# Performance work log

Hardware: AMD Instinct MI355X
Metric: run time of the kernel (lower is better)

Reference implementation:

```python
import jax, jax.numpy as jnp
import numpy as np

K = 3        # kernel_size
STRIDE = 1
PAD = 1
DIL = 1


def setup_inputs() -> dict:
    key = jax.random.key(0)
    ks = jax.random.split(key, 5)
    B, C, H, W, O = 4, 64, 128, 128, 64
    x = jax.random.normal(ks[0], (B, C, H, W), jnp.float32)
    # small offset-conv weights -> offsets of a few pixels (realistic trained regime)
    offset_w = jax.random.normal(ks[1], (2 * K * K, C, K, K), jnp.float32) * 0.01
    offset_b = jax.random.normal(ks[2], (2 * K * K,), jnp.float32) * 0.01
    weight = jax.random.normal(ks[3], (O, C, K, K), jnp.float32)
    bias = jax.random.normal(ks[4], (O,), jnp.float32)
    return {"x": x, "offset_w": offset_w, "offset_b": offset_b,
            "weight": weight, "bias": bias}


def _conv2d(x, w, b):
    y = jax.lax.conv_general_dilated(
        x, w, window_strides=(STRIDE, STRIDE),
        padding=[(PAD, PAD), (PAD, PAD)],
        dimension_numbers=("NCHW", "OIHW", "NCHW"))
    return y + b[None, :, None, None]


def _deform_conv2d(x, offset, weight, bias):
    B, C, H, W = x.shape
    O = weight.shape[0]
    KK = K * K
    Ho, Wo = offset.shape[2], offset.shape[3]
    # offset channels ordered (y, x) per kernel tap: [B, KK, 2, Ho, Wo]
    off = offset.reshape(B, KK, 2, Ho, Wo)
    kyy, kxx = jnp.meshgrid(jnp.arange(K) * DIL, jnp.arange(K) * DIL, indexing="ij")
    kyy = kyy.reshape(KK).astype(x.dtype)
    kxx = kxx.reshape(KK).astype(x.dtype)
    base_y = (jnp.arange(Ho) * STRIDE - PAD).astype(x.dtype)
    base_x = (jnp.arange(Wo) * STRIDE - PAD).astype(x.dtype)
    # sampling positions [B, KK, Ho, Wo]
    py = base_y[None, None, :, None] + kyy[None, :, None, None] + off[:, :, 0]
    px = base_x[None, None, None, :] + kxx[None, :, None, None] + off[:, :, 1]

    y0 = jnp.floor(py); x0 = jnp.floor(px)
    y1 = y0 + 1.0;      x1 = x0 + 1.0
    wy1 = py - y0; wy0 = 1.0 - wy1
    wx1 = px - x0; wx0 = 1.0 - wx1

    xf = x.reshape(B, C, H * W)

    def corner(yc, xc):
        valid = (yc >= 0) & (yc < H) & (xc >= 0) & (xc < W)  # zero padding outside
        idx = (jnp.clip(yc, 0, H - 1) * W + jnp.clip(xc, 0, W - 1)).astype(jnp.int32)
        g = jax.vmap(lambda xb, ib: xb[:, ib.reshape(-1)])(xf, idx)  # [B, C, KK*Ho*Wo]
        g = g.reshape(B, C, KK, Ho, Wo)
        return g * valid[:, None].astype(x.dtype)

    val = (corner(y0, x0) * (wy0 * wx0)[:, None]
         + corner(y0, x1) * (wy0 * wx1)[:, None]
         + corner(y1, x0) * (wy1 * wx0)[:, None]
         + corner(y1, x1) * (wy1 * wx1)[:, None])  # [B, C, KK, Ho, Wo]

    out = jnp.einsum("bckhw,ock->bohw", val, weight.reshape(O, C, KK))
    return out + bias[None, :, None, None]


def reference(x, offset_w, offset_b, weight, bias):
    offset = _conv2d(x, offset_w, offset_b)
    return _deform_conv2d(x, offset, weight, bias)
```

## Files before the change

kernel.cpp:

```cpp
#include <hip/hip_runtime.h>

#define B_   4
#define C_   64
#define O_   64
#define H_   128
#define W_   128
#define HW_  (H_ * W_)
#define KK_  9
#define M_   18

typedef short  short8  __attribute__((ext_vector_type(8)));
typedef float  floatx4 __attribute__((ext_vector_type(4)));
typedef unsigned short ushort4v __attribute__((ext_vector_type(4)));
typedef unsigned short ushort8v __attribute__((ext_vector_type(8)));

static __device__ __forceinline__ unsigned short f2bf(float f) {
    unsigned int u = __float_as_uint(f);
    u += 0x7FFFu + ((u >> 16) & 1u);
    return (unsigned short)(u >> 16);
}
static __device__ __forceinline__ float bf2f(unsigned short s) {
    return __uint_as_float((unsigned int)s << 16);
}

__global__ __launch_bounds__(256) void prep(
        const float* __restrict__ x, const float* __restrict__ w,
        const float* __restrict__ ow, unsigned short* __restrict__ xT,
        unsigned short* __restrict__ wtbf, unsigned short* __restrict__ owtbf) {
    const int blk = blockIdx.x;
    if (blk < 512) {
        __shared__ unsigned short T[128][72];
        const int tid = threadIdx.x;
        const int y = blk & (H_ - 1);
        const int b = blk >> 7;
        const float* xby = x + (size_t)b * C_ * HW_ + y * W_;
        for (int i = tid; i < C_ * W_; i += 256) {
            const int c = i >> 7, xc = i & 127;
            T[xc][c] = f2bf(xby[(size_t)c * HW_ + xc]);
        }
        __syncthreads();
        unsigned short* dst = xT + (size_t)b * (4 * HW_ * 16) + y * (W_ * 16);
        for (int j = tid; j < 2048; j += 256) {
            const int g  = j >> 9;
            const int x8 = (j >> 2) & 127;
            const int c0 = (j & 3) * 4;
            const ushort4v pk = *(const ushort4v*)&T[x8][g * 16 + c0];
            *(ushort4v*)&dst[(size_t)g * (HW_ * 16) + x8 * 16 + c0] = pk;
        }
    } else if (blk < 530) {
        const int i = (blk - 512) * 256 + threadIdx.x;
        const int lane = i & 63, rest = i >> 6;
        const int ot = rest & 3, cks = rest >> 2;
        const int chunk = cks / 6, ks = cks % 6;
        const int o = ot * 16 + (lane & 15);
        const int kbase = chunk * 192 + ks * 32 + (lane >> 4) * 8;
        ushort8v pk;
        #pragma unroll
        for (int j = 0; j < 8; ++j) {
            const int k = kbase + j;
            pk[j] = f2bf(w[o * 576 + (k & 63) * 9 + (k >> 6)]);
        }
        *(ushort8v*)&wtbf[(size_t)i * 8] = pk;
    } else {
        const int i = (blk - 530) * 256 + threadIdx.x;
        const int lane = i & 63, rest = i >> 6;
        const int tile = rest & 1, tks = rest >> 1;
        const int tap = tks >> 1, ks = tks & 1;
        const int m = tile * 16 + (lane & 15);
        const int cb = ks * 32 + (lane >> 4) * 8;
        ushort8v pk;
        #pragma unroll
        for (int j = 0; j < 8; ++j)
            pk[j] = (m < M_) ? f2bf(ow[m * 576 + (cb + j) * 9 + tap])
                             : (unsigned short)0;
        *(ushort8v*)&owtbf[(size_t)i * 8] = pk;
    }
}

__global__ __launch_bounds__(256, 5) void dcn_fused(
        const unsigned short* __restrict__ xT,
        const unsigned short* __restrict__ owtbf, const float* __restrict__ ob,
        const unsigned short* __restrict__ wtbf, const float* __restrict__ bias,
        float* __restrict__ out) {
    __shared__ union {
        unsigned short P[3][66][72];
        struct {
            unsigned short vals[64][192];
            float offs[M_ * 64];
        } bv;
        float ep[4][16][65];
    } u;

    const int tid    = threadIdx.x;
    const int lane   = tid & 63;
    const int wslot  = __builtin_amdgcn_readfirstlane(tid >> 6);
    const int lane15 = lane & 15;
    const int quad   = lane >> 4;

    const int g    = blockIdx.x;
    const int xcd  = g & 7;
    const int slot = g >> 3;
    const int ho   = xcd * 16 + (slot >> 3);
    const int b    = (slot >> 1) & 3;
    const int wo_base = (slot & 1) << 6;

    const unsigned short* xTb = xT + (size_t)b * (4 * HW_ * 16);

    #pragma unroll
    for (int it = 0; it < 3; ++it) {
        const int t  = it * 4 + wslot;
        const int ky = t >> 2, cgp = t & 3;
        const int y  = ho - 1 + ky;
        const bool yv = (unsigned)y < (unsigned)H_;
        const unsigned short* src = xTb + (size_t)cgp * (HW_ * 16) + y * (W_ * 16);
        #pragma unroll
        for (int pass = 0; pass < 2; ++pass) {
            const int r = pass * 64 + lane;
            if (r < 66) {
                const int cx = wo_base + r - 1;
                ushort8v p0 = {0, 0, 0, 0, 0, 0, 0, 0};
                ushort8v p1 = {0, 0, 0, 0, 0, 0, 0, 0};
                if (yv && (unsigned)cx < (unsigned)W_) {
                    p0 = *(const ushort8v*)&src[cx * 16];
                    p1 = *(const ushort8v*)&src[cx * 16 + 8];
                }
                *(ushort8v*)&u.P[ky][r][cgp * 16]     = p0;
                *(ushort8v*)&u.P[ky][r][cgp * 16 + 8] = p1;
            }
        }
    }
    __syncthreads();

    {
        floatx4 oa0 = (floatx4){0.f, 0.f, 0.f, 0.f};
        floatx4 oa1 = (floatx4){0.f, 0.f, 0.f, 0.f};
        const int pxt = wslot;
        #pragma unroll
        for (int ky = 0; ky < 3; ++ky) {
            #pragma unroll
            for (int kx = 0; kx < 3; ++kx) {
                const int tap = ky * 3 + kx;
                #pragma unroll
                for (int ks = 0; ks < 2; ++ks) {
                    const int kk = ks * 32 + quad * 8;
                    const short8 af =
                        *(const short8*)&u.P[ky][pxt * 16 + lane15 + kx][kk];
                    const int fb = ((tap * 2 + ks) * 2) * 64 + lane;
                    const short8 bf0 = *(const short8*)&owtbf[(size_t)fb * 8];
                    const short8 bf1 =
                        *(const short8*)&owtbf[(size_t)(fb + 64) * 8];
                    oa0 = __builtin_amdgcn_mfma_f32_16x16x32_bf16(af, bf0, oa0, 0, 0, 0);
                    oa1 = __builtin_amdgcn_mfma_f32_16x16x32_bf16(af, bf1, oa1, 0, 0, 0);
                }
            }
        }
        __syncthreads();
        *(floatx4*)&u.bv.offs[lane15 * 64 + pxt * 16 + quad * 4] = oa0;
        if (lane15 < 2)
            *(floatx4*)&u.bv.offs[(16 + lane15) * 64 + pxt * 16 + quad * 4] = oa1;
    }
    __syncthreads();

    const int obase = wslot * 16;
    const int cg    = lane & 3;
    const int px16  = lane >> 2;
    floatx4 acc[4];
    #pragma unroll
    for (int t = 0; t < 4; ++t) acc[t] = (floatx4){0.f, 0.f, 0.f, 0.f};
    const unsigned short* xTw = xTb + (size_t)wslot * (HW_ * 16);

    for (int chunk = 0; chunk < 3; ++chunk) {
        #pragma unroll
        for (int tl = 0; tl < 3; ++tl) {
            const int k  = chunk * 3 + tl;
            const int ky = k / 3, kx = k % 3;
            const float oby = ob[2 * k], obx = ob[2 * k + 1];
            #pragma unroll
            for (int pxt = 0; pxt < 4; ++pxt) {
                const int px = pxt * 16 + px16;
                const float offy = u.bv.offs[(2 * k)     * 64 + px] + oby;
                const float offx = u.bv.offs[(2 * k + 1) * 64 + px] + obx;
                const float py  = (float)(ho - 1 + ky) + offy;
                const float pxx = (float)(wo_base - 1 + kx + px) + offx;
                const float fy = floorf(py), fx = floorf(pxx);
                const int y0 = (int)fy, x0 = (int)fx;
                const int y1 = y0 + 1,  x1 = x0 + 1;
                const float wy1 = py - fy,  wy0 = 1.f - wy1;
                const float wx1 = pxx - fx, wx0 = 1.f - wx1;
                const bool y0v = (unsigned)y0 < (unsigned)H_;
                const bool y1v = (unsigned)y1 < (unsigned)H_;
                const bool x0v = (unsigned)x0 < (unsigned)W_;
                const bool x1v = (unsigned)x1 < (unsigned)W_;
                const float w00 = (y0v && x0v) ? wy0 * wx0 : 0.f;
                const float w01 = (y0v && x1v) ? wy0 * wx1 : 0.f;
                const float w10 = (y1v && x0v) ? wy1 * wx0 : 0.f;
                const float w11 = (y1v && x1v) ? wy1 * wx1 : 0.f;
                const int ry0 = min(max(y0, 0), H_ - 1);
                const int ry1 = min(max(y1, 0), H_ - 1);
                const int cx0 = min(max(x0, 0), W_ - 1);
                const int cx1 = min(max(x1, 0), W_ - 1);
                const int a00 = (ry0 * W_ + cx0) * 16 + cg * 4;
                const int a01 = (ry0 * W_ + cx1) * 16 + cg * 4;
                const int a10 = (ry1 * W_ + cx0) * 16 + cg * 4;
                const int a11 = (ry1 * W_ + cx1) * 16 + cg * 4;
                const ushort4v q00 = *(const ushort4v*)&xTw[a00];
                const ushort4v q01 = *(const ushort4v*)&xTw[a01];
                const ushort4v q10 = *(const ushort4v*)&xTw[a10];
                const ushort4v q11 = *(const ushort4v*)&xTw[a11];
                ushort4v pk;
                #pragma unroll
                for (int q = 0; q < 4; ++q) {
                    const float val = bf2f(q00[q]) * w00 + bf2f(q01[q]) * w01
                                    + bf2f(q10[q]) * w10 + bf2f(q11[q]) * w11;
                    pk[q] = f2bf(val);
                }
                const int cidx =
                    tl * 8 + (((wslot << 1) + (cg >> 1)) ^ (px & 7));
                *(ushort4v*)&u.bv.vals[px][cidx * 8 + (cg & 1) * 4] = pk;
            }
        }
        __syncthreads();

        #pragma unroll
        for (int ks = 0; ks < 6; ++ks) {
            const short8 bfrag = *(const short8*)
                &wtbf[(size_t)(((chunk * 6 + ks) * 4 + wslot) * 64 + lane) * 8];
            const int ca  = (ks * 4 + quad) >> 3;
            const int cbr = ((ks * 4 + quad) & 7) ^ (lane15 & 7);
            #pragma unroll
            for (int t = 0; t < 4; ++t) {
                const int row = t * 16 + lane15;
                const short8 afrag =
                    *(const short8*)&u.bv.vals[row][(ca * 8 + cbr) * 8];
                acc[t] = __builtin_amdgcn_mfma_f32_16x16x32_bf16(
                             afrag, bfrag, acc[t], 0, 0, 0);
            }
        }
        __syncthreads();
    }

    #pragma unroll
    for (int t = 0; t < 4; ++t)
        #pragma unroll
        for (int r = 0; r < 4; ++r)
            u.ep[wslot][lane15][t * 16 + quad * 4 + r] = acc[t][r];
    __syncthreads();
    #pragma unroll
    for (int oi = 0; oi < 16; ++oi) {
        const int o = obase + oi;
        out[(size_t)(b * O_ + o) * HW_ + ho * W_ + wo_base + lane] =
            u.ep[wslot][oi][lane] + bias[o];
    }
}

extern "C" void kernel_launch(void* const* d_in, const int* in_sizes, int n_in,
                              void* d_out, int out_size, void* d_ws, size_t ws_size,
                              hipStream_t stream) {
    const float* x    = (const float*)d_in[0];
    const float* ow   = (const float*)d_in[1];
    const float* ob   = (const float*)d_in[2];
    const float* w    = (const float*)d_in[3];
    const float* bias = (const float*)d_in[4];
    float* out = (float*)d_out;

    unsigned short* wtbf  = (unsigned short*)d_ws;
    unsigned short* owtbf = wtbf + 4608 * 8;
    unsigned short* xT    = owtbf + 2304 * 8;

    prep<<<539, 256, 0, stream>>>(x, w, ow, xT, wtbf, owtbf);
    dcn_fused<<<B_ * H_ * (W_ / 64), 256, 0, stream>>>(xT, owtbf, ob, wtbf, bias, out);
}
```

Measured before the change: 117.9 us.

## Make each wave own a 16-pixel slice to drop inter-wave barriers

Reassigns the bilinear sampling and MFMA work so that each wavefront handles its own 16 output pixels across all 64 channels and all 64 output channels, instead of splitting work by channel group and output-channel group. The offsets, sampled values and epilogue staging then stay within a wave's private shared-memory rows, which removes most of the per-chunk __syncthreads barriers and the separate epilogue buffer. Offset bias is folded in once before the store. The launch bound drops from 5 to 4 waves per EU, and each wave now reads all four B-fragments from global memory per k-step, which raises global weight traffic and register pressure.

```diff
diff --git a/kernel.cpp b/kernel.cpp
--- a/kernel.cpp
+++ b/kernel.cpp
@@ -77,7 +77,7 @@
     }
 }
 
-__global__ __launch_bounds__(256, 5) void dcn_fused(
+__global__ __launch_bounds__(256, 4) void dcn_fused(
         const unsigned short* __restrict__ xT,
         const unsigned short* __restrict__ owtbf, const float* __restrict__ ob,
         const unsigned short* __restrict__ wtbf, const float* __restrict__ bias,
@@ -86,9 +86,8 @@
         unsigned short P[3][66][72];
         struct {
             unsigned short vals[64][192];
-            float offs[M_ * 64];
+            float offs[4][M_][16];
         } bv;
-        float ep[4][16][65];
     } u;
 
     const int tid    = threadIdx.x;
@@ -131,9 +130,9 @@
     }
     __syncthreads();
 
+    floatx4 oa0 = (floatx4){0.f, 0.f, 0.f, 0.f};
+    floatx4 oa1 = (floatx4){0.f, 0.f, 0.f, 0.f};
     {
-        floatx4 oa0 = (floatx4){0.f, 0.f, 0.f, 0.f};
-        floatx4 oa1 = (floatx4){0.f, 0.f, 0.f, 0.f};
         const int pxt = wslot;
         #pragma unroll
         for (int ky = 0; ky < 3; ++ky) {
@@ -154,59 +153,66 @@
                 }
             }
         }
-        __syncthreads();
-        *(floatx4*)&u.bv.offs[lane15 * 64 + pxt * 16 + quad * 4] = oa0;
-        if (lane15 < 2)
-            *(floatx4*)&u.bv.offs[(16 + lane15) * 64 + pxt * 16 + quad * 4] = oa1;
     }
     __syncthreads();
 
-    const int obase = wslot * 16;
-    const int cg    = lane & 3;
-    const int px16  = lane >> 2;
+    {
+        const float ob0 = ob[lane15];
+        #pragma unroll
+        for (int r = 0; r < 4; ++r) oa0[r] += ob0;
+        *(floatx4*)&u.bv.offs[wslot][lane15][quad * 4] = oa0;
+        if (lane15 < 2) {
+            const float ob1 = ob[16 + lane15];
+            #pragma unroll
+            for (int r = 0; r < 4; ++r) oa1[r] += ob1;
+            *(floatx4*)&u.bv.offs[wslot][16 + lane15][quad * 4] = oa1;
+        }
+    }
+
+    const int cg4  = lane & 3;
+    const int px16 = lane >> 2;
+    const int row  = wslot * 16 + px16;
     floatx4 acc[4];
     #pragma unroll
     for (int t = 0; t < 4; ++t) acc[t] = (floatx4){0.f, 0.f, 0.f, 0.f};
-    const unsigned short* xTw = xTb + (size_t)wslot * (HW_ * 16);
 
     for (int chunk = 0; chunk < 3; ++chunk) {
         #pragma unroll
         for (int tl = 0; tl < 3; ++tl) {
             const int k  = chunk * 3 + tl;
             const int ky = k / 3, kx = k % 3;
-            const float oby = ob[2 * k], obx = ob[2 * k + 1];
-            #pragma unroll
-            for (int pxt = 0; pxt < 4; ++pxt) {
-                const int px = pxt * 16 + px16;
-                const float offy = u.bv.offs[(2 * k)     * 64 + px] + oby;
-                const float offx = u.bv.offs[(2 * k + 1) * 64 + px] + obx;
-                const float py  = (float)(ho - 1 + ky) + offy;
-                const float pxx = (float)(wo_base - 1 + kx + px) + offx;
-                const float fy = floorf(py), fx = floorf(pxx);
-                const int y0 = (int)fy, x0 = (int)fx;
-                const int y1 = y0 + 1,  x1 = x0 + 1;
-                const float wy1 = py - fy,  wy0 = 1.f - wy1;
-                const float wx1 = pxx - fx, wx0 = 1.f - wx1;
-                const bool y0v = (unsigned)y0 < (unsigned)H_;
-                const bool y1v = (unsigned)y1 < (unsigned)H_;
-                const bool x0v = (unsigned)x0 < (unsigned)W_;
-                const bool x1v = (unsigned)x1 < (unsigned)W_;
-                const float w00 = (y0v && x0v) ? wy0 * wx0 : 0.f;
-                const float w01 = (y0v && x1v) ? wy0 * wx1 : 0.f;
-                const float w10 = (y1v && x0v) ? wy1 * wx0 : 0.f;
-                const float w11 = (y1v && x1v) ? wy1 * wx1 : 0.f;
-                const int ry0 = min(max(y0, 0), H_ - 1);
-                const int ry1 = min(max(y1, 0), H_ - 1);
-                const int cx0 = min(max(x0, 0), W_ - 1);
-                const int cx1 = min(max(x1, 0), W_ - 1);
-                const int a00 = (ry0 * W_ + cx0) * 16 + cg * 4;
-                const int a01 = (ry0 * W_ + cx1) * 16 + cg * 4;
-                const int a10 = (ry1 * W_ + cx0) * 16 + cg * 4;
-                const int a11 = (ry1 * W_ + cx1) * 16 + cg * 4;
-                const ushort4v q00 = *(const ushort4v*)&xTw[a00];
-                const ushort4v q01 = *(const ushort4v*)&xTw[a01];
-                const ushort4v q10 = *(const ushort4v*)&xTw[a10];
-                const ushort4v q11 = *(const ushort4v*)&xTw[a11];
+            const float offy = u.bv.offs[wslot][2 * k][px16];
+            const float offx = u.bv.offs[wslot][2 * k + 1][px16];
+            const float py  = (float)(ho - 1 + ky) + offy;
+            const float pxx = (float)(wo_base - 1 + kx + wslot * 16 + px16) + offx;
+            const float fy = floorf(py), fx = floorf(pxx);
+            const int y0 = (int)fy, x0 = (int)fx;
+            const int y1 = y0 + 1,  x1 = x0 + 1;
+            const float wy1 = py - fy,  wy0 = 1.f - wy1;
+            const float wx1 = pxx - fx, wx0 = 1.f - wx1;
+            const bool y0v = (unsigned)y0 < (unsigned)H_;
+            const bool y1v = (unsigned)y1 < (unsigned)H_;
+            const bool x0v = (unsigned)x0 < (unsigned)W_;
+            const bool x1v = (unsigned)x1 < (unsigned)W_;
+            const float w00 = (y0v && x0v) ? wy0 * wx0 : 0.f;
+            const float w01 = (y0v && x1v) ? wy0 * wx1 : 0.f;
+            const float w10 = (y1v && x0v) ? wy1 * wx0 : 0.f;
+            const float w11 = (y1v && x1v) ? wy1 * wx1 : 0.f;
+            const int ry0 = min(max(y0, 0), H_ - 1);
+            const int ry1 = min(max(y1, 0), H_ - 1);
+            const int cx0 = min(max(x0, 0), W_ - 1);
+            const int cx1 = min(max(x1, 0), W_ - 1);
+            const int b00 = (ry0 * W_ + cx0) * 16 + cg4 * 4;
+            const int b01 = (ry0 * W_ + cx1) * 16 + cg4 * 4;
+            const int b10 = (ry1 * W_ + cx0) * 16 + cg4 * 4;
+            const int b11 = (ry1 * W_ + cx1) * 16 + cg4 * 4;
+            #pragma unroll
+            for (int cgrp = 0; cgrp < 4; ++cgrp) {
+                const unsigned short* xp = xTb + (size_t)cgrp * (HW_ * 16);
+                const ushort4v q00 = *(const ushort4v*)&xp[b00];
+                const ushort4v q01 = *(const ushort4v*)&xp[b01];
+                const ushort4v q10 = *(const ushort4v*)&xp[b10];
+                const ushort4v q11 = *(const ushort4v*)&xp[b11];
                 ushort4v pk;
                 #pragma unroll
                 for (int q = 0; q < 4; ++q) {
@@ -215,41 +221,41 @@
                     pk[q] = f2bf(val);
                 }
                 const int cidx =
-                    tl * 8 + (((wslot << 1) + (cg >> 1)) ^ (px & 7));
-                *(ushort4v*)&u.bv.vals[px][cidx * 8 + (cg & 1) * 4] = pk;
-            }
-        }
-        __syncthreads();
+                    tl * 8 + (((cgrp << 1) + (cg4 >> 1)) ^ (px16 & 7));
+                *(ushort4v*)&u.bv.vals[row][cidx * 8 + (cg4 & 1) * 4] = pk;
+            }
+        }
 
         #pragma unroll
         for (int ks = 0; ks < 6; ++ks) {
-            const short8 bfrag = *(const short8*)
-                &wtbf[(size_t)(((chunk * 6 + ks) * 4 + wslot) * 64 + lane) * 8];
-            const int ca  = (ks * 4 + quad) >> 3;
-            const int cbr = ((ks * 4 + quad) & 7) ^ (lane15 & 7);
+            const int c16 = ks * 4 + quad;
+            const int ca  = c16 >> 3;
+            const int cbr = (c16 & 7) ^ (lane15 & 7);
+            const short8 afrag = *(const short8*)
+                &u.bv.vals[wslot * 16 + lane15][(ca * 8 + cbr) * 8];
             #pragma unroll
             for (int t = 0; t < 4; ++t) {
-                const int row = t * 16 + lane15;
-                const short8 afrag =
-                    *(const short8*)&u.bv.vals[row][(ca * 8 + cbr) * 8];
+                const short8 bfrag = *(const short8*)
+                    &wtbf[(size_t)(((chunk * 6 + ks) * 4 + t) * 64 + lane) * 8];
                 acc[t] = __builtin_amdgcn_mfma_f32_16x16x32_bf16(
                              afrag, bfrag, acc[t], 0, 0, 0);
             }
         }
-        __syncthreads();
-    }
-
+    }
+
+    float* epw = (float*)&u.bv.vals[wslot * 16][0];
     #pragma unroll
     for (int t = 0; t < 4; ++t)
         #pragma unroll
         for (int r = 0; r < 4; ++r)
-            u.ep[wslot][lane15][t * 16 + quad * 4 + r] = acc[t][r];
-    __syncthreads();
-    #pragma unroll
-    for (int oi = 0; oi < 16; ++oi) {
-        const int o = obase + oi;
-        out[(size_t)(b * O_ + o) * HW_ + ho * W_ + wo_base + lane] =
-            u.ep[wslot][oi][lane] + bias[o];
+            epw[(t * 16 + lane15) * 17 + quad * 4 + r] = acc[t][r];
+
+    const int wo = wo_base + wslot * 16 + lane15;
+    #pragma unroll
+    for (int i = 0; i < 16; ++i) {
+        const int o = i * 4 + quad;
+        out[(size_t)(b * O_ + o) * HW_ + ho * W_ + wo] =
+            epw[o * 17 + lane15] + bias[o];
     }
 }
 
```

Result: faster. 115.5 us (-2.0%).
